# Kernel optimization log

Hardware: AMD Instinct MI355X
Metric: run time of the kernel (lower is better)

Reference implementation:

```python
import math
import jax, jax.numpy as jnp
import numpy as np

B, L, C, E, H, NL, WIN, VOCAB, NC = 2, 1024, 4, 256, 8, 2, 256, 25, 10
HID = 2 * E                      # FFN expansion=2
IN_PAIR = C * (WIN + 1)          # PairwiseContextProjector MLP in_dim


def _sinusoidal_pe(max_len, dim):
    pos = np.arange(max_len, dtype=np.float32)[:, None]
    div = np.exp(np.arange(0, dim, 2, dtype=np.float32) * (-math.log(10000.0) / dim))
    pe = np.zeros((max_len, dim), np.float32)
    pe[:, 0::2] = np.sin(pos * div)
    pe[:, 1::2] = np.cos(pos * div)
    return jnp.asarray(pe)


def setup_inputs() -> dict:
    key = jax.random.key(0)
    ks = iter(jax.random.split(key, 64))
    def rn(shape, scale):
        return jax.random.normal(next(ks), shape, jnp.float32) * scale
    inp = {}
    inp['tokens'] = jax.random.randint(next(ks), (B, L), 0, VOCAB, dtype=jnp.int32)
    inp['x_pairwise'] = rn((B, C, L, L), 1.0)
    inp['bias'] = rn((B, H, L, L), 1.0)
    inp['mask'] = jnp.ones((B, L), jnp.float32)
    inp['token_emb'] = rn((VOCAB, E), 0.02).at[0].set(0.0)  # padding_idx=0
    inp['pe'] = _sinusoidal_pe(L, E)
    inp['pair_w1'] = rn((IN_PAIR, E), IN_PAIR ** -0.5)
    inp['pair_b1'] = jnp.zeros((E,), jnp.float32)
    inp['pair_w2'] = rn((E, E), E ** -0.5)
    inp['pair_b2'] = jnp.zeros((E,), jnp.float32)
    inp['ln1_g'] = jnp.ones((NL, E), jnp.float32)
    inp['ln1_b'] = jnp.zeros((NL, E), jnp.float32)
    for nm in ('wq', 'wk', 'wv', 'wo'):
        inp[nm] = rn((NL, E, E), E ** -0.5)
    for nm in ('bq', 'bk', 'bv', 'bo'):
        inp[nm] = jnp.zeros((NL, E), jnp.float32)
    inp['gate'] = jnp.full((NL, H), 0.5, jnp.float32)   # bias_gate init 0.5
    inp['ln2_g'] = jnp.ones((NL, E), jnp.float32)
    inp['ln2_b'] = jnp.zeros((NL, E), jnp.float32)
    inp['fw1'] = rn((NL, E, HID), E ** -0.5)
    inp['fb1'] = jnp.zeros((NL, HID), jnp.float32)
    inp['fw2'] = rn((NL, HID, E), HID ** -0.5)
    inp['fb2'] = jnp.zeros((NL, E), jnp.float32)
    inp['hln_g'] = jnp.ones((E,), jnp.float32)
    inp['hln_b'] = jnp.zeros((E,), jnp.float32)
    inp['hw1'] = rn((E, E), E ** -0.5)
    inp['hb1'] = jnp.zeros((E,), jnp.float32)
    inp['hw2'] = rn((E, NC), E ** -0.5)
    inp['hb2'] = jnp.zeros((NC,), jnp.float32)
    return inp


def _ln(x, g, b):
    m = x.mean(-1, keepdims=True)
    v = ((x - m) ** 2).mean(-1, keepdims=True)
    return (x - m) / jnp.sqrt(v + 1e-5) * g + b


def _gelu(x):
    return jax.nn.gelu(x, approximate=False)  # torch nn.GELU default = exact erf


def _forward(tokens, x_pairwise, bias, mask, token_emb, pe,
             pair_w1, pair_b1, pair_w2, pair_b2,
             ln1_g, ln1_b, wq, bq, wk, bk, wv, bv, wo, bo, gate,
             ln2_g, ln2_b, fw1, fb1, fw2, fb2,
             hln_g, hln_b, hw1, hb1, hw2, hb2):
    Bx, Lx = tokens.shape
    half = WIN // 2
    padded = jnp.pad(x_pairwise, ((0, 0), (0, 0), (0, 0), (half, half)))
    idx = (jnp.arange(Lx)[:, None] + jnp.arange(WIN + 1)[None, :])[None, None]
    win = jnp.take_along_axis(padded, idx, axis=3)          # [B,C,L,W+1]
    flat = win.transpose(0, 2, 1, 3).reshape(Bx, Lx, C * (WIN + 1))
    pair_ctx = jnp.maximum(flat @ pair_w1 + pair_b1, 0.0) @ pair_w2 + pair_b2

    # SequenceEmbedding + pairwise context
    x = token_emb[tokens] + pe[None, :Lx] + pair_ctx         # [B,L,E]

    D = E // H
    scale = D ** -0.5
    key_bias = (1.0 - mask)[:, None, None, :] * (-10000.0)   # [B,1,1,L]
    for i in range(NL):
        # BiasedMultiHeadAttention (pre-norm + residual)
        xn = _ln(x, ln1_g[i], ln1_b[i])
        Q = (xn @ wq[i] + bq[i]).reshape(Bx, Lx, H, D)
        K = (xn @ wk[i] + bk[i]).reshape(Bx, Lx, H, D)
        V = (xn @ wv[i] + bv[i]).reshape(Bx, Lx, H, D)
        logits = jnp.einsum('blhd,bmhd->bhlm', Q, K) * scale
        logits = logits + gate[i][None, :, None, None] * bias + key_bias
        attn = jax.nn.softmax(logits, axis=-1)
        attn = jnp.nan_to_num(attn) * mask[:, None, :, None]
        out = jnp.einsum('bhlm,bmhd->blhd', attn, V).reshape(Bx, Lx, E)
        out = out * mask[..., None]
        x = x + out @ wo[i] + bo[i]
        # FeedForwardNetwork: x + W2(GELU(W1(LN(x))))
        x = x + _gelu(_ln(x, ln2_g[i], ln2_b[i]) @ fw1[i] + fb1[i]) @ fw2[i] + fb2[i]

    # masked mean pool + ClassificationHead
    pooled = (x * mask[..., None]).sum(1) / jnp.maximum(mask.sum(1, keepdims=True), 1.0)
    h = _ln(pooled, hln_g, hln_b)
    return _gelu(h @ hw1 + hb1) @ hw2 + hb2                  # [B, NC]


def reference(tokens, x_pairwise, bias, mask, token_emb, pe,
              pair_w1, pair_b1, pair_w2, pair_b2,
              ln1_g, ln1_b, wq, bq, wk, bk, wv, bv, wo, bo, gate,
              ln2_g, ln2_b, fw1, fb1, fw2, fb2,
              hln_g, hln_b, hw1, hb1, hw2, hb2):
    return _forward(tokens, x_pairwise, bias, mask, token_emb, pe,
                    pair_w1, pair_b1, pair_w2, pair_b2,
                    ln1_g, ln1_b, wq, bq, wk, bk, wv, bv, wo, bo, gate,
                    ln2_g, ln2_b, fw1, fb1, fw2, fb2,
                    hln_g, hln_b, hw1, hb1, hw2, hb2)
```

## Files before the change

kernel.cpp:

```cpp
#include <hip/hip_runtime.h>
#include <math.h>

#define BB     2
#define LL     1024
#define CC     4
#define EE     256
#define HH     8
#define DD     32
#define NLAYER 2
#define W1N    257
#define INPAIR 1028
#define KP1    1056
#define HIDN   512
#define NCN    10
#define SCALEF 0.17677669529663687f

typedef short bf16x8 __attribute__((ext_vector_type(8)));
typedef float f32x4  __attribute__((ext_vector_type(4)));
typedef unsigned short u16x4 __attribute__((ext_vector_type(4)));
typedef unsigned short u16x8 __attribute__((ext_vector_type(8)));

__device__ __forceinline__ float gelu_f(float x) {
    return 0.5f * x * (1.0f + erff(x * 0.7071067811865475f));
}
__device__ __forceinline__ unsigned short f2bf(float f) {
    unsigned u = __float_as_uint(f);
    u += 0x7fffu + ((u >> 16) & 1u);
    return (unsigned short)(u >> 16);
}

struct PrepDesc {
    const float* src[14];
    int K[14];
    int N[14];
    unsigned long long dst[14];
};

__global__ __launch_bounds__(256) void prep_w(PrepDesc pd, unsigned short* __restrict__ wt)
{
    const int mi = blockIdx.y;
    const int k8 = blockIdx.x;
    const int K = pd.K[mi], N = pd.N[mi];
    const int Kp = (K + 31) & ~31;
    if (k8 * 8 >= Kp) return;
    const float* src = pd.src[mi];
    unsigned short* dst = wt + pd.dst[mi];
    for (int n = threadIdx.x; n < N; n += 256) {
        u16x8 o;
        #pragma unroll
        for (int j = 0; j < 8; ++j) {
            int k = k8 * 8 + j;
            float v = (k < K) ? src[(size_t)k * N + n] : 0.f;
            o[j] = f2bf(v);
        }
        *(u16x8*)(dst + ((size_t)k8 * N + n) * 8) = o;
    }
}

__global__ __launch_bounds__(256) void gather_flat(
    const float* __restrict__ xp, unsigned short* __restrict__ flat)
{
    const int row = blockIdx.x;
    const int b = row >> 10, l = row & 1023;
    const float* base = xp + (size_t)b * CC * LL * LL + (size_t)l * LL;
    for (int kp = threadIdx.x; kp < KP1; kp += 256) {
        float v = 0.f;
        if (kp < INPAIR) {
            int c = kp / W1N;
            int w = kp - c * W1N;
            int col = l + w - 128;
            if (col >= 0 && col < LL) v = base[(size_t)c * LL * LL + col];
        }
        flat[(size_t)row * KP1 + kp] = f2bf(v);
    }
}

__global__ __launch_bounds__(256) void ln_bf16(
    const float* __restrict__ x, const float* __restrict__ g,
    const float* __restrict__ bt, unsigned short* __restrict__ out)
{
    const int row = blockIdx.x * 4 + (threadIdx.x >> 6);
    const int lane = threadIdx.x & 63;
    float4 v = *(const float4*)(x + (size_t)row * EE + lane * 4);
    float s = v.x + v.y + v.z + v.w;
    #pragma unroll
    for (int m = 1; m < 64; m <<= 1) s += __shfl_xor(s, m, 64);
    const float mu = s * (1.0f / 256.0f);
    float q2 = 0.f, d;
    d = v.x - mu; q2 += d * d; d = v.y - mu; q2 += d * d;
    d = v.z - mu; q2 += d * d; d = v.w - mu; q2 += d * d;
    #pragma unroll
    for (int m = 1; m < 64; m <<= 1) q2 += __shfl_xor(q2, m, 64);
    const float rstd = rsqrtf(q2 * (1.0f / 256.0f) + 1e-5f);
    float4 gg = *(const float4*)(g + lane * 4);
    float4 bb = *(const float4*)(bt + lane * 4);
    u16x4 o;
    o[0] = f2bf((v.x - mu) * rstd * gg.x + bb.x);
    o[1] = f2bf((v.y - mu) * rstd * gg.y + bb.y);
    o[2] = f2bf((v.z - mu) * rstd * gg.z + bb.z);
    o[3] = f2bf((v.w - mu) * rstd * gg.w + bb.w);
    *(u16x4*)(out + (size_t)row * EE + lane * 4) = o;
}

template<int KP, int EPI>
__global__ __launch_bounds__(256) void gemm_mfma(
    const unsigned short* __restrict__ A,
    const unsigned short* wt0, const float* b0, void* o0,
    const unsigned short* wt1, const float* b1, void* o1,
    const unsigned short* wt2, const float* b2, void* o2,
    int N,
    const int* __restrict__ tokens, const float* __restrict__ temb,
    const float* __restrict__ pe)
{
    const int t = threadIdx.x;
    const int w = t >> 6, lane = t & 63;
    const int m0 = blockIdx.x * 64 + w * 16;
    const int n0 = blockIdx.y * 16;
    const unsigned short* WT; const float* bias; void* out;
    if (blockIdx.z == 0)      { WT = wt0; bias = b0; out = o0; }
    else if (blockIdx.z == 1) { WT = wt1; bias = b1; out = o1; }
    else                      { WT = wt2; bias = b2; out = o2; }

    const int q = lane >> 4, li = lane & 15;
    const unsigned short* ap = A + (size_t)(m0 + li) * KP + q * 8;
    const unsigned short* bp = WT + ((size_t)q * N + n0 + li) * 8;
    f32x4 acc = {0.f, 0.f, 0.f, 0.f};
    for (int ks = 0; ks < KP / 32; ++ks) {
        bf16x8 av = *(const bf16x8*)(ap + ks * 32);
        bf16x8 bv = *(const bf16x8*)(bp + (size_t)ks * 32 * N);
        acc = __builtin_amdgcn_mfma_f32_16x16x32_bf16(av, bv, acc, 0, 0, 0);
    }

    const int colg = n0 + li;
    const float bb = bias[colg];
    const int rbase = m0 + q * 4;
    #pragma unroll
    for (int r = 0; r < 4; ++r) {
        const int row = rbase + r;
        float v = acc[r] + bb;
        if constexpr (EPI == 0) {
            int b = row >> 10, l = row & 1023;
            int h = colg >> 5, d = colg & 31;
            int bh = b * HH + h;
            unsigned short* op = (unsigned short*)out;
            if (blockIdx.z == 0)
                op[((size_t)bh * LL + l) * DD + d] = f2bf(v);
            else if (blockIdx.z == 1)
                op[(size_t)bh * 32768 + (size_t)(d >> 3) * 8192 + (size_t)l * 8 + (d & 7)] = f2bf(v);
            else
                op[(size_t)bh * 32768 + (size_t)(l >> 3) * 256 + (size_t)d * 8 + (l & 7)] = f2bf(v);
        } else if constexpr (EPI == 1) {
            float* op = (float*)out;
            op[(size_t)row * N + colg] += v;
        } else if constexpr (EPI == 2) {
            ((unsigned short*)out)[(size_t)row * N + colg] = f2bf(gelu_f(v));
        } else if constexpr (EPI == 3) {
            ((unsigned short*)out)[(size_t)row * N + colg] = f2bf(fmaxf(v, 0.f));
        } else {
            int tok = tokens[row];
            v += temb[(size_t)tok * EE + colg] + pe[(size_t)(row & 1023) * EE + colg];
            ((float*)out)[(size_t)row * EE + colg] = v;
        }
    }
}

__global__ __launch_bounds__(256) void attn_mfma(
    const unsigned short* __restrict__ qb,
    const unsigned short* __restrict__ kswz,
    const unsigned short* __restrict__ vswz,
    const float* __restrict__ bias, const float* __restrict__ mask,
    const float* __restrict__ gate, unsigned short* __restrict__ aob)
{
    __shared__ unsigned short Pbuf[4][16][72];
    const int t = threadIdx.x;
    const int wq = t >> 6, lane = t & 63;
    const int li = lane & 15, qd = lane >> 4;
    const int h = blockIdx.y, b = blockIdx.z;
    const int bh = b * HH + h;
    const int q0 = blockIdx.x * 64 + wq * 16;
    const float gh = gate[h];

    const bf16x8 qfrag = *(const bf16x8*)(qb + ((size_t)bh * LL + q0 + li) * DD + qd * 8);

    const unsigned short* kbase = kswz + (size_t)bh * 32768 + (size_t)qd * 8192 + (size_t)li * 8;
    const unsigned short* vbase = vswz + (size_t)bh * 32768 + (size_t)qd * 256 + (size_t)li * 8;
    const float* bp0 = bias + ((size_t)bh * LL + q0 + qd * 4) * LL + li;
    const float* mkp = mask + (size_t)b * LL + li;

    float mrun[4], lrun[4];
    f32x4 o0 = {0.f, 0.f, 0.f, 0.f}, o1 = {0.f, 0.f, 0.f, 0.f};
    #pragma unroll
    for (int r = 0; r < 4; ++r) { mrun[r] = -3.0e38f; lrun[r] = 0.f; }

    float bpre[4][4], kbpre[4];
    #pragma unroll
    for (int ms = 0; ms < 4; ++ms) {
        kbpre[ms] = mkp[ms * 16];
        #pragma unroll
        for (int r = 0; r < 4; ++r) bpre[ms][r] = bp0[(size_t)r * LL + ms * 16];
    }

    for (int mt = 0; mt < 16; ++mt) {
        const int m0 = mt * 64;
        f32x4 S[4];
        #pragma unroll
        for (int ms = 0; ms < 4; ++ms) {
            bf16x8 kf = *(const bf16x8*)(kbase + (size_t)(m0 + ms * 16) * 8);
            f32x4 z = {0.f, 0.f, 0.f, 0.f};
            S[ms] = __builtin_amdgcn_mfma_f32_16x16x32_bf16(qfrag, kf, z, 0, 0, 0);
        }
        float bc[4][4], kbc[4];
        #pragma unroll
        for (int ms = 0; ms < 4; ++ms) {
            kbc[ms] = (1.0f - kbpre[ms]) * (-10000.0f);
            #pragma unroll
            for (int r = 0; r < 4; ++r) bc[ms][r] = bpre[ms][r];
        }
        if (mt < 15) {
            #pragma unroll
            for (int ms = 0; ms < 4; ++ms) {
                kbpre[ms] = mkp[m0 + 64 + ms * 16];
                #pragma unroll
                for (int r = 0; r < 4; ++r) bpre[ms][r] = bp0[(size_t)r * LL + m0 + 64 + ms * 16];
            }
        }
        float lg[4][4];
        #pragma unroll
        for (int ms = 0; ms < 4; ++ms)
            #pragma unroll
            for (int r = 0; r < 4; ++r)
                lg[ms][r] = fmaf(S[ms][r], SCALEF, fmaf(gh, bc[ms][r], kbc[ms]));

        float rmax[4];
        #pragma unroll
        for (int r = 0; r < 4; ++r) {
            rmax[r] = fmaxf(fmaxf(lg[0][r], lg[1][r]), fmaxf(lg[2][r], lg[3][r]));
        }
        #pragma unroll
        for (int bit = 1; bit < 16; bit <<= 1) {
            #pragma unroll
            for (int r = 0; r < 4; ++r) rmax[r] = fmaxf(rmax[r], __shfl_xor(rmax[r], bit, 64));
        }
        float alpha[4], rsum[4];
        #pragma unroll
        for (int r = 0; r < 4; ++r) {
            float nm = fmaxf(mrun[r], rmax[r]);
            alpha[r] = expf(mrun[r] - nm);
            mrun[r] = nm;
        }
        float p[4][4];
        #pragma unroll
        for (int r = 0; r < 4; ++r) rsum[r] = 0.f;
        #pragma unroll
        for (int ms = 0; ms < 4; ++ms)
            #pragma unroll
            for (int r = 0; r < 4; ++r) {
                p[ms][r] = expf(lg[ms][r] - mrun[r]);
                rsum[r] += p[ms][r];
            }
        #pragma unroll
        for (int bit = 1; bit < 16; bit <<= 1) {
            #pragma unroll
            for (int r = 0; r < 4; ++r) rsum[r] += __shfl_xor(rsum[r], bit, 64);
        }
        #pragma unroll
        for (int r = 0; r < 4; ++r) lrun[r] = lrun[r] * alpha[r] + rsum[r];
        #pragma unroll
        for (int r = 0; r < 4; ++r) { o0[r] *= alpha[r]; o1[r] *= alpha[r]; }
        #pragma unroll
        for (int ms = 0; ms < 4; ++ms)
            #pragma unroll
            for (int r = 0; r < 4; ++r)
                Pbuf[wq][qd * 4 + r][ms * 16 + li] = f2bf(p[ms][r]);
        #pragma unroll
        for (int c = 0; c < 2; ++c) {
            bf16x8 pa = *(const bf16x8*)&Pbuf[wq][li][c * 32 + qd * 8];
            bf16x8 vf0 = *(const bf16x8*)(vbase + (size_t)((m0 >> 3) + c * 4) * 256);
            bf16x8 vf1 = *(const bf16x8*)(vbase + (size_t)((m0 >> 3) + c * 4) * 256 + 16 * 8);
            o0 = __builtin_amdgcn_mfma_f32_16x16x32_bf16(pa, vf0, o0, 0, 0, 0);
            o1 = __builtin_amdgcn_mfma_f32_16x16x32_bf16(pa, vf1, o1, 0, 0, 0);
        }
    }
    #pragma unroll
    for (int r = 0; r < 4; ++r) {
        const int row = q0 + qd * 4 + r;
        const float mq = mask[(size_t)b * LL + row];
        const float sc = (lrun[r] > 0.f ? 1.0f / lrun[r] : 0.f) * mq * mq;
        const size_t obase = ((size_t)b * LL + row) * EE + h * DD;
        aob[obase + li]      = f2bf(o0[r] * sc);
        aob[obase + 16 + li] = f2bf(o1[r] * sc);
    }
}

__global__ __launch_bounds__(256) void pool_part(
    const float* __restrict__ x, const float* __restrict__ mask,
    float* __restrict__ part, float* __restrict__ pmask)
{
    const int ch = blockIdx.x, b = blockIdx.y, t = threadIdx.x;
    const int l0 = ch * 64;
    float s = 0.f, ms = 0.f;
    for (int i = 0; i < 64; ++i) {
        int l = l0 + i;
        float mm = mask[b * LL + l];
        s = fmaf(x[((size_t)(b * LL + l)) * EE + t], mm, s);
        ms += mm;
    }
    part[(size_t)(b * 16 + ch) * EE + t] = s;
    if (t == 0) pmask[b * 16 + ch] = ms;
}

__global__ __launch_bounds__(256) void head_kernel(
    const float* __restrict__ part, const float* __restrict__ pmask,
    const float* __restrict__ hg, const float* __restrict__ hb,
    const float* __restrict__ w1, const float* __restrict__ b1,
    const float* __restrict__ w2, const float* __restrict__ b2,
    float* __restrict__ outp)
{
    __shared__ float pn[EE];
    __shared__ float g1s[EE];
    __shared__ float red[4];
    const int t = threadIdx.x;
    for (int b = 0; b < BB; ++b) {
        float v = 0.f, msum = 0.f;
        #pragma unroll
        for (int c = 0; c < 16; ++c) {
            v += part[(size_t)(b * 16 + c) * EE + t];
            msum += pmask[b * 16 + c];
        }
        v = v / fmaxf(msum, 1.0f);
        float s = v;
        #pragma unroll
        for (int mm = 1; mm < 64; mm <<= 1) s += __shfl_xor(s, mm, 64);
        if ((t & 63) == 0) red[t >> 6] = s;
        __syncthreads();
        const float mu = (red[0] + red[1] + red[2] + red[3]) * (1.0f / 256.0f);
        __syncthreads();
        float d = v - mu;
        float q2 = d * d;
        #pragma unroll
        for (int mm = 1; mm < 64; mm <<= 1) q2 += __shfl_xor(q2, mm, 64);
        if ((t & 63) == 0) red[t >> 6] = q2;
        __syncthreads();
        const float var = (red[0] + red[1] + red[2] + red[3]) * (1.0f / 256.0f);
        const float rstd = rsqrtf(var + 1e-5f);
        pn[t] = d * rstd * hg[t] + hb[t];
        __syncthreads();
        float acc = b1[t];
        for (int k = 0; k < EE; ++k) acc = fmaf(pn[k], w1[k * EE + t], acc);
        g1s[t] = gelu_f(acc);
        __syncthreads();
        if (t < NCN) {
            float a2 = b2[t];
            for (int k = 0; k < EE; ++k) a2 = fmaf(g1s[k], w2[k * NCN + t], a2);
            outp[b * NCN + t] = a2;
        }
        __syncthreads();
    }
}

extern "C" void kernel_launch(void* const* d_in, const int* in_sizes, int n_in,
                              void* d_out, int out_size, void* d_ws, size_t ws_size,
                              hipStream_t stream) {
    const int*   tokens = (const int*)  d_in[0];
    const float* xp     = (const float*)d_in[1];
    const float* bias   = (const float*)d_in[2];
    const float* mask   = (const float*)d_in[3];
    const float* temb   = (const float*)d_in[4];
    const float* pe     = (const float*)d_in[5];
    const float* pw1    = (const float*)d_in[6];
    const float* pb1    = (const float*)d_in[7];
    const float* pw2    = (const float*)d_in[8];
    const float* pb2    = (const float*)d_in[9];
    const float* ln1g   = (const float*)d_in[10];
    const float* ln1b   = (const float*)d_in[11];
    const float* wq     = (const float*)d_in[12];
    const float* wk     = (const float*)d_in[13];
    const float* wv     = (const float*)d_in[14];
    const float* wo     = (const float*)d_in[15];
    const float* bq     = (const float*)d_in[16];
    const float* bk     = (const float*)d_in[17];
    const float* bv     = (const float*)d_in[18];
    const float* bo     = (const float*)d_in[19];
    const float* gate   = (const float*)d_in[20];
    const float* ln2g   = (const float*)d_in[21];
    const float* ln2b   = (const float*)d_in[22];
    const float* fw1    = (const float*)d_in[23];
    const float* fb1    = (const float*)d_in[24];
    const float* fw2    = (const float*)d_in[25];
    const float* fb2    = (const float*)d_in[26];
    const float* hlng   = (const float*)d_in[27];
    const float* hlnb   = (const float*)d_in[28];
    const float* hw1    = (const float*)d_in[29];
    const float* hb1    = (const float*)d_in[30];
    const float* hw2    = (const float*)d_in[31];
    const float* hb2    = (const float*)d_in[32];

    float* ws = (float*)d_ws;
    const size_t NTOK = (size_t)BB * LL * EE;
    float* x      = ws;
    float* part   = ws + NTOK;
    float* pmaskp = part + 32 * EE;
    unsigned short* usp = (unsigned short*)(pmaskp + 64);
    usp = (unsigned short*)(((size_t)usp + 15) & ~(size_t)15);
    unsigned short* qb16 = usp;
    unsigned short* kswz = qb16 + NTOK;
    unsigned short* vswz = kswz + NTOK;
    unsigned short* xn   = vswz + NTOK;
    unsigned short* aob  = xn + NTOK;
    unsigned short* ffh  = aob + NTOK;
    unsigned short* ph   = ffh + (size_t)BB * LL * HIDN;
    unsigned short* flat = ph + NTOK;
    unsigned short* wt   = flat + (size_t)BB * LL * KP1;

    const size_t OFF_PW1 = 0;
    const size_t OFF_PW2 = 270336;
    const size_t OFF_QKVO = 335872;
    const size_t OFF_FW1 = 860160;
    const size_t OFF_FW2 = 1122304;

    PrepDesc pd;
    pd.src[0] = pw1;  pd.K[0] = INPAIR; pd.N[0] = EE;  pd.dst[0] = OFF_PW1;
    pd.src[1] = pw2;  pd.K[1] = EE;     pd.N[1] = EE;  pd.dst[1] = OFF_PW2;
    for (int l = 0; l < 2; ++l) {
        const float* srcs[4] = {wq + l * EE * EE, wk + l * EE * EE,
                                wv + l * EE * EE, wo + l * EE * EE};
        for (int wch = 0; wch < 4; ++wch) {
            int mi = 2 + l * 4 + wch;
            pd.src[mi] = srcs[wch]; pd.K[mi] = EE; pd.N[mi] = EE;
            pd.dst[mi] = OFF_QKVO + (size_t)(l * 4 + wch) * 65536;
        }
    }
    for (int l = 0; l < 2; ++l) {
        pd.src[10 + l] = fw1 + (size_t)l * EE * HIDN;
        pd.K[10 + l] = EE;  pd.N[10 + l] = HIDN;
        pd.dst[10 + l] = OFF_FW1 + (size_t)l * 131072;
        pd.src[12 + l] = fw2 + (size_t)l * HIDN * EE;
        pd.K[12 + l] = HIDN; pd.N[12 + l] = EE;
        pd.dst[12 + l] = OFF_FW2 + (size_t)l * 131072;
    }
    prep_w<<<dim3(KP1 / 8, 14), dim3(256), 0, stream>>>(pd, wt);

    gather_flat<<<dim3(2048), dim3(256), 0, stream>>>(xp, flat);
    gemm_mfma<KP1, 3><<<dim3(32, 16, 1), dim3(256), 0, stream>>>(
        flat, wt + OFF_PW1, pb1, ph, nullptr, nullptr, nullptr,
        nullptr, nullptr, nullptr, EE, nullptr, nullptr, nullptr);
    gemm_mfma<EE, 4><<<dim3(32, 16, 1), dim3(256), 0, stream>>>(
        ph, wt + OFF_PW2, pb2, x, nullptr, nullptr, nullptr,
        nullptr, nullptr, nullptr, EE, tokens, temb, pe);

    for (int i = 0; i < NLAYER; ++i) {
        ln_bf16<<<dim3(512), dim3(256), 0, stream>>>(x, ln1g + i * EE, ln1b + i * EE, xn);
        gemm_mfma<EE, 0><<<dim3(32, 16, 3), dim3(256), 0, stream>>>(
            xn,
            wt + OFF_QKVO + (size_t)(i * 4 + 0) * 65536, bq + i * EE, qb16,
            wt + OFF_QKVO + (size_t)(i * 4 + 1) * 65536, bk + i * EE, kswz,
            wt + OFF_QKVO + (size_t)(i * 4 + 2) * 65536, bv + i * EE, vswz,
            EE, nullptr, nullptr, nullptr);
        attn_mfma<<<dim3(16, HH, BB), dim3(256), 0, stream>>>(
            qb16, kswz, vswz, bias, mask, gate + i * HH, aob);
        gemm_mfma<EE, 1><<<dim3(32, 16, 1), dim3(256), 0, stream>>>(
            aob, wt + OFF_QKVO + (size_t)(i * 4 + 3) * 65536, bo + i * EE, x,
            nullptr, nullptr, nullptr, nullptr, nullptr, nullptr,
            EE, nullptr, nullptr, nullptr);
        ln_bf16<<<dim3(512), dim3(256), 0, stream>>>(x, ln2g + i * EE, ln2b + i * EE, xn);
        gemm_mfma<EE, 2><<<dim3(32, 32, 1), dim3(256), 0, stream>>>(
            xn, wt + OFF_FW1 + (size_t)i * 131072, fb1 + i * HIDN, ffh,
            nullptr, nullptr, nullptr, nullptr, nullptr, nullptr,
            HIDN, nullptr, nullptr, nullptr);
        gemm_mfma<HIDN, 1><<<dim3(32, 16, 1), dim3(256), 0, stream>>>(
            ffh, wt + OFF_FW2 + (size_t)i * 131072, fb2 + i * EE, x,
            nullptr, nullptr, nullptr, nullptr, nullptr, nullptr,
            EE, nullptr, nullptr, nullptr);
    }

    pool_part<<<dim3(16, BB), dim3(256), 0, stream>>>(x, mask, part, pmaskp);
    head_kernel<<<dim3(1), dim3(256), 0, stream>>>(
        part, pmaskp, hlng, hlnb, hw1, hb1, hw2, hb2, (float*)d_out);

    (void)in_sizes; (void)n_in; (void)out_size; (void)ws_size;
}
```

Before: 353.0 us.

## Split attention over key chunks with a merge kernel; parallelize head over batch

Attention now splits the 1024 keys into four 256-key chunks, so the grid grows from 256 to 1024 blocks. Each block writes unnormalized partial outputs plus running max and sum statistics, and a new merge kernel combines them flash-decoding style. The goal is to fill more of the GPU's compute units and hide bias-load latency. The cost is an extra launch and fp32 partial-output traffic of about 8 MB per layer. The head kernel also runs one block per batch, and its second matmul becomes a shuffle reduction instead of a 10-thread serial loop.

Result: faster. 332.0 us (-5.9%).

```diff
diff --git a/kernel.cpp b/kernel.cpp
--- a/kernel.cpp
+++ b/kernel.cpp
@@ -164,12 +164,14 @@
     }
 }
 
-__global__ __launch_bounds__(256) void attn_mfma(
+__global__ __launch_bounds__(256, 4) void attn_part_mfma(
     const unsigned short* __restrict__ qb,
     const unsigned short* __restrict__ kswz,
     const unsigned short* __restrict__ vswz,
     const float* __restrict__ bias, const float* __restrict__ mask,
-    const float* __restrict__ gate, unsigned short* __restrict__ aob)
+    const float* __restrict__ gate,
+    float* __restrict__ Opart, float* __restrict__ statsM,
+    float* __restrict__ statsL)
 {
     __shared__ unsigned short Pbuf[4][16][72];
     const int t = threadIdx.x;
@@ -177,7 +179,9 @@
     const int li = lane & 15, qd = lane >> 4;
     const int h = blockIdx.y, b = blockIdx.z;
     const int bh = b * HH + h;
-    const int q0 = blockIdx.x * 64 + wq * 16;
+    const int qt = blockIdx.x & 15, mc = blockIdx.x >> 4;
+    const int q0 = qt * 64 + wq * 16;
+    const int mbase = mc * 256;
     const float gh = gate[h];
 
     const bf16x8 qfrag = *(const bf16x8*)(qb + ((size_t)bh * LL + q0 + li) * DD + qd * 8);
@@ -195,13 +199,13 @@
     float bpre[4][4], kbpre[4];
     #pragma unroll
     for (int ms = 0; ms < 4; ++ms) {
-        kbpre[ms] = mkp[ms * 16];
-        #pragma unroll
-        for (int r = 0; r < 4; ++r) bpre[ms][r] = bp0[(size_t)r * LL + ms * 16];
-    }
-
-    for (int mt = 0; mt < 16; ++mt) {
-        const int m0 = mt * 64;
+        kbpre[ms] = mkp[mbase + ms * 16];
+        #pragma unroll
+        for (int r = 0; r < 4; ++r) bpre[ms][r] = bp0[(size_t)r * LL + mbase + ms * 16];
+    }
+
+    for (int mtt = 0; mtt < 4; ++mtt) {
+        const int m0 = mbase + mtt * 64;
         f32x4 S[4];
         #pragma unroll
         for (int ms = 0; ms < 4; ++ms) {
@@ -216,7 +220,7 @@
             #pragma unroll
             for (int r = 0; r < 4; ++r) bc[ms][r] = bpre[ms][r];
         }
-        if (mt < 15) {
+        if (mtt < 3) {
             #pragma unroll
             for (int ms = 0; ms < 4; ++ms) {
                 kbpre[ms] = mkp[m0 + 64 + ms * 16];
@@ -233,9 +237,8 @@
 
         float rmax[4];
         #pragma unroll
-        for (int r = 0; r < 4; ++r) {
+        for (int r = 0; r < 4; ++r)
             rmax[r] = fmaxf(fmaxf(lg[0][r], lg[1][r]), fmaxf(lg[2][r], lg[3][r]));
-        }
         #pragma unroll
         for (int bit = 1; bit < 16; bit <<= 1) {
             #pragma unroll
@@ -281,15 +284,45 @@
             o1 = __builtin_amdgcn_mfma_f32_16x16x32_bf16(pa, vf1, o1, 0, 0, 0);
         }
     }
+    const size_t rowg0 = (size_t)(mc * 2 + b) * LL;
     #pragma unroll
     for (int r = 0; r < 4; ++r) {
         const int row = q0 + qd * 4 + r;
-        const float mq = mask[(size_t)b * LL + row];
-        const float sc = (lrun[r] > 0.f ? 1.0f / lrun[r] : 0.f) * mq * mq;
-        const size_t obase = ((size_t)b * LL + row) * EE + h * DD;
-        aob[obase + li]      = f2bf(o0[r] * sc);
-        aob[obase + 16 + li] = f2bf(o1[r] * sc);
-    }
+        const size_t rg = rowg0 + row;
+        Opart[rg * EE + h * DD + li]      = o0[r];
+        Opart[rg * EE + h * DD + 16 + li] = o1[r];
+        if (li == 0) {
+            statsM[rg * HH + h] = mrun[r];
+            statsL[rg * HH + h] = lrun[r];
+        }
+    }
+}
+
+__global__ __launch_bounds__(256) void attn_merge(
+    const float* __restrict__ Opart, const float* __restrict__ statsM,
+    const float* __restrict__ statsL, const float* __restrict__ mask,
+    unsigned short* __restrict__ aob)
+{
+    const int row = blockIdx.x;
+    const int e = threadIdx.x;
+    const int h = e >> 5;
+    float m_[4];
+    float M = -3.0e38f;
+    #pragma unroll
+    for (int mc = 0; mc < 4; ++mc) {
+        m_[mc] = statsM[((size_t)mc * 2048 + row) * HH + h];
+        M = fmaxf(M, m_[mc]);
+    }
+    float Lsum = 0.f, V = 0.f;
+    #pragma unroll
+    for (int mc = 0; mc < 4; ++mc) {
+        float sc = expf(m_[mc] - M);
+        Lsum = fmaf(statsL[((size_t)mc * 2048 + row) * HH + h], sc, Lsum);
+        V = fmaf(Opart[((size_t)mc * 2048 + row) * EE + e], sc, V);
+    }
+    const float mq = mask[row];
+    const float r = (Lsum > 0.f ? V / Lsum : 0.f) * mq * mq;
+    aob[(size_t)row * EE + e] = f2bf(r);
 }
 
 __global__ __launch_bounds__(256) void pool_part(
@@ -299,6 +332,7 @@
     const int ch = blockIdx.x, b = blockIdx.y, t = threadIdx.x;
     const int l0 = ch * 64;
     float s = 0.f, ms = 0.f;
+    #pragma unroll 4
     for (int i = 0; i < 64; ++i) {
         int l = l0 + i;
         float mm = mask[b * LL + l];
@@ -317,45 +351,55 @@
     float* __restrict__ outp)
 {
     __shared__ float pn[EE];
-    __shared__ float g1s[EE];
     __shared__ float red[4];
+    __shared__ float wred[4][NCN];
+    const int b = blockIdx.x;
     const int t = threadIdx.x;
-    for (int b = 0; b < BB; ++b) {
-        float v = 0.f, msum = 0.f;
-        #pragma unroll
-        for (int c = 0; c < 16; ++c) {
-            v += part[(size_t)(b * 16 + c) * EE + t];
-            msum += pmask[b * 16 + c];
-        }
-        v = v / fmaxf(msum, 1.0f);
-        float s = v;
-        #pragma unroll
-        for (int mm = 1; mm < 64; mm <<= 1) s += __shfl_xor(s, mm, 64);
-        if ((t & 63) == 0) red[t >> 6] = s;
-        __syncthreads();
-        const float mu = (red[0] + red[1] + red[2] + red[3]) * (1.0f / 256.0f);
-        __syncthreads();
-        float d = v - mu;
-        float q2 = d * d;
-        #pragma unroll
-        for (int mm = 1; mm < 64; mm <<= 1) q2 += __shfl_xor(q2, mm, 64);
-        if ((t & 63) == 0) red[t >> 6] = q2;
-        __syncthreads();
-        const float var = (red[0] + red[1] + red[2] + red[3]) * (1.0f / 256.0f);
-        const float rstd = rsqrtf(var + 1e-5f);
-        pn[t] = d * rstd * hg[t] + hb[t];
-        __syncthreads();
-        float acc = b1[t];
-        for (int k = 0; k < EE; ++k) acc = fmaf(pn[k], w1[k * EE + t], acc);
-        g1s[t] = gelu_f(acc);
-        __syncthreads();
-        if (t < NCN) {
-            float a2 = b2[t];
-            for (int k = 0; k < EE; ++k) a2 = fmaf(g1s[k], w2[k * NCN + t], a2);
-            outp[b * NCN + t] = a2;
-        }
-        __syncthreads();
-    }
+    const int wv = t >> 6, lane = t & 63;
+
+    float v = 0.f, msum = 0.f;
+    #pragma unroll
+    for (int c = 0; c < 16; ++c) {
+        v += part[(size_t)(b * 16 + c) * EE + t];
+        msum += pmask[b * 16 + c];
+    }
+    v = v / fmaxf(msum, 1.0f);
+    float s = v;
+    #pragma unroll
+    for (int mm = 1; mm < 64; mm <<= 1) s += __shfl_xor(s, mm, 64);
+    if (lane == 0) red[wv] = s;
+    __syncthreads();
+    const float mu = (red[0] + red[1] + red[2] + red[3]) * (1.0f / 256.0f);
+    __syncthreads();
+    float d = v - mu;
+    float q2 = d * d;
+    #pragma unroll
+    for (int mm = 1; mm < 64; mm <<= 1) q2 += __shfl_xor(q2, mm, 64);
+    if (lane == 0) red[wv] = q2;
+    __syncthreads();
+    const float var = (red[0] + red[1] + red[2] + red[3]) * (1.0f / 256.0f);
+    const float rstd = rsqrtf(var + 1e-5f);
+    pn[t] = d * rstd * hg[t] + hb[t];
+    __syncthreads();
+    float acc = b1[t];
+    #pragma unroll 8
+    for (int k = 0; k < EE; ++k) acc = fmaf(pn[k], w1[k * EE + t], acc);
+    const float g = gelu_f(acc);
+    float contrib[NCN];
+    #pragma unroll
+    for (int c = 0; c < NCN; ++c) contrib[c] = g * w2[(size_t)t * NCN + c];
+    #pragma unroll
+    for (int mm = 1; mm < 64; mm <<= 1) {
+        #pragma unroll
+        for (int c = 0; c < NCN; ++c) contrib[c] += __shfl_xor(contrib[c], mm, 64);
+    }
+    if (lane == 0) {
+        #pragma unroll
+        for (int c = 0; c < NCN; ++c) wred[wv][c] = contrib[c];
+    }
+    __syncthreads();
+    if (t < NCN)
+        outp[b * NCN + t] = b2[t] + wred[0][t] + wred[1][t] + wred[2][t] + wred[3][t];
 }
 
 extern "C" void kernel_launch(void* const* d_in, const int* in_sizes, int n_in,
@@ -400,7 +444,10 @@
     float* x      = ws;
     float* part   = ws + NTOK;
     float* pmaskp = part + 32 * EE;
-    unsigned short* usp = (unsigned short*)(pmaskp + 64);
+    float* Opart  = pmaskp + 64;
+    float* statsM = Opart + 4 * NTOK;
+    float* statsL = statsM + 65536;
+    unsigned short* usp = (unsigned short*)(statsL + 65536);
     usp = (unsigned short*)(((size_t)usp + 15) & ~(size_t)15);
     unsigned short* qb16 = usp;
     unsigned short* kswz = qb16 + NTOK;
@@ -456,8 +503,9 @@
             wt + OFF_QKVO + (size_t)(i * 4 + 1) * 65536, bk + i * EE, kswz,
             wt + OFF_QKVO + (size_t)(i * 4 + 2) * 65536, bv + i * EE, vswz,
             EE, nullptr, nullptr, nullptr);
-        attn_mfma<<<dim3(16, HH, BB), dim3(256), 0, stream>>>(
-            qb16, kswz, vswz, bias, mask, gate + i * HH, aob);
+        attn_part_mfma<<<dim3(64, HH, BB), dim3(256), 0, stream>>>(
+            qb16, kswz, vswz, bias, mask, gate + i * HH, Opart, statsM, statsL);
+        attn_merge<<<dim3(2048), dim3(256), 0, stream>>>(Opart, statsM, statsL, mask, aob);
         gemm_mfma<EE, 1><<<dim3(32, 16, 1), dim3(256), 0, stream>>>(
             aob, wt + OFF_QKVO + (size_t)(i * 4 + 3) * 65536, bo + i * EE, x,
             nullptr, nullptr, nullptr, nullptr, nullptr, nullptr,
@@ -474,7 +522,7 @@
     }
 
     pool_part<<<dim3(16, BB), dim3(256), 0, stream>>>(x, mask, part, pmaskp);
-    head_kernel<<<dim3(1), dim3(256), 0, stream>>>(
+    head_kernel<<<dim3(BB), dim3(256), 0, stream>>>(
         part, pmaskp, hlng, hlnb, hw1, hb1, hw2, hb2, (float*)d_out);
 
     (void)in_sizes; (void)n_in; (void)out_size; (void)ws_size;
```
